# Optimization experiments

Hardware: AMD Instinct MI355X
Metric: run time of the kernel (lower is better)

## Reference

```python
import jax, jax.numpy as jnp
import numpy as np

B, N, C = 64, 1024, 128
H1, H2 = 256, 128
ACTION = N


def _xavier(key, shape):
    lim = float(np.sqrt(6.0 / (shape[0] + shape[1])))
    return jax.random.uniform(key, shape, jnp.float32, -lim, lim)


def setup_inputs() -> dict:
    key = jax.random.key(0)
    ks = jax.random.split(key, 16)
    node_features = jax.random.normal(ks[0], (B, N, 3), jnp.float32)
    adjacency_matrix = jax.random.randint(ks[1], (B, N, N), 0, 2).astype(jnp.int32)
    return {
        "node_features": node_features,
        "adjacency_matrix": adjacency_matrix,
        "W_in": _xavier(ks[2], (3, C)),
        "a_src": _xavier(ks[3], (C, 1)),
        "a_dst": _xavier(ks[4], (C, 1)),
        "a_src2": _xavier(ks[5], (C, 1)),
        "a_dst2": _xavier(ks[6], (C, 1)),
        "W1": _xavier(ks[7], (C, H1)),
        "b1": jnp.zeros((H1,), jnp.float32),
        "W2": _xavier(ks[8], (H1, H2)),
        "b2": jnp.zeros((H2,), jnp.float32),
        "Wpi": _xavier(ks[9], (H2, ACTION)),
        "bpi": jnp.zeros((ACTION,), jnp.float32),
        "Wv": _xavier(ks[10], (H2, 1)),
        "bv": jnp.zeros((1,), jnp.float32),
    }


def _gat_layer(x, mask, a_src, a_dst):
    # x: [B,N,C]; mask: [B,N,N] bool
    ai = jnp.squeeze(x @ a_src, -1)  # [B,N] score of node as source (i)
    aj = jnp.squeeze(x @ a_dst, -1)  # [B,N] score of node as dest (j)
    e = ai[:, :, None] + aj[:, None, :]  # [B,N,N]
    e = jnp.where(e > 0, e, 0.2 * e)  # leaky_relu(0.2)
    e = jnp.where(mask, e, jnp.float32(-1e9))  # masked_fill(-inf)
    alpha = jax.nn.softmax(e, axis=-1)  # [B,N,N]
    out = jnp.einsum("bij,bjc->bic", alpha, x)  # weighted neighbor aggregation
    return jax.nn.relu(out)


def reference(node_features, adjacency_matrix, W_in, a_src, a_dst, a_src2, a_dst2,
              W1, b1, W2, b2, Wpi, bpi, Wv, bv):
    mask = adjacency_matrix > 0
    x = node_features @ W_in  # [B,N,C], no bias
    x = _gat_layer(x, mask, a_src, a_dst)
    x = _gat_layer(x, mask, a_src2, a_dst2)
    x = jnp.mean(x, axis=1)  # [B,C]
    x = jax.nn.relu(x @ W1 + b1)
    x = jax.nn.relu(x @ W2 + b2)
    pi = jax.nn.softmax(x @ Wpi + bpi, axis=1)
    v = x @ Wv + bv
    return (pi, v)
```

## Files before the change

kernel.cpp:

```cpp
#include <hip/hip_runtime.h>

#define Bn 64
#define Nn 1024
#define Cc 128

typedef _Float16 h8 __attribute__((ext_vector_type(8)));
typedef float f4v __attribute__((ext_vector_type(4)));
typedef unsigned long long u64;

__global__ __launch_bounds__(256) void k_feat(
    const float* __restrict__ nf, const float* __restrict__ Win,
    const float* __restrict__ asrc, const float* __restrict__ adst,
    _Float16* __restrict__ X0, float* __restrict__ ai, float* __restrict__ aj,
    float* __restrict__ E, float* __restrict__ G, float* __restrict__ F, float* __restrict__ H) {
  int g = blockIdx.x; int b = g >> 7; int n0 = (g & 127) << 3;
  int t = threadIdx.x; int c = t >> 1; int h = t & 1;
  float w0 = Win[c], w1 = Win[Cc + c], w2 = Win[2 * Cc + c];
  float as_ = asrc[c], ad = adst[c];
  float ps[4], pd[4];
  _Float16 hv[4];
  #pragma unroll
  for (int r = 0; r < 4; r++) {
    int n = n0 + (h << 2) + r;
    const float* p = nf + ((size_t)(b << 10) + n) * 3;
    float x = p[0] * w0 + p[1] * w1 + p[2] * w2;
    hv[r] = (_Float16)x; ps[r] = x * as_; pd[r] = x * ad;
  }
  *(uint2*)(X0 + ((size_t)b << 17) + ((size_t)(g & 127) << 10) + (c << 3) + (h << 2)) = *(uint2*)hv;
  #pragma unroll
  for (int off = 32; off > 1; off >>= 1) {
    #pragma unroll
    for (int r = 0; r < 4; r++) { ps[r] += __shfl_down(ps[r], off, 64); pd[r] += __shfl_down(pd[r], off, 64); }
  }
  __shared__ float red[4][2][4][2];
  int lane = t & 63, wv = t >> 6;
  if (lane < 2) {
    #pragma unroll
    for (int r = 0; r < 4; r++) { red[wv][lane][r][0] = ps[r]; red[wv][lane][r][1] = pd[r]; }
  }
  __syncthreads();
  if (t < 8) {
    int hh = t >> 2, r = t & 3;
    float sa = 0.f, sd = 0.f;
    #pragma unroll
    for (int w = 0; w < 4; w++) { sa += red[w][hh][r][0]; sd += red[w][hh][r][1]; }
    int gi = (b << 10) + n0 + t;
    ai[gi] = sa; aj[gi] = sd;
    E[gi] = __expf(sa); G[gi] = __expf(0.2f * sa);
    F[gi] = __expf(sd); H[gi] = __expf(0.2f * sd);
  }
}

__global__ __launch_bounds__(256) void k_scores2(
    const _Float16* __restrict__ X1,
    const float* __restrict__ asrc, const float* __restrict__ adst,
    float* __restrict__ ai, float* __restrict__ aj,
    float* __restrict__ E, float* __restrict__ G, float* __restrict__ F, float* __restrict__ H) {
  int g = blockIdx.x; int b = g >> 7; int n0 = (g & 127) << 3;
  int t = threadIdx.x; int c = t >> 1; int h = t & 1;
  float as_ = asrc[c], ad = adst[c];
  uint2 raw = *(const uint2*)(X1 + ((size_t)b << 17) + ((size_t)(g & 127) << 10) + (c << 3) + (h << 2));
  const _Float16* hp = (const _Float16*)&raw;
  float ps[4], pd[4];
  #pragma unroll
  for (int r = 0; r < 4; r++) { float x = (float)hp[r]; ps[r] = x * as_; pd[r] = x * ad; }
  #pragma unroll
  for (int off = 32; off > 1; off >>= 1) {
    #pragma unroll
    for (int r = 0; r < 4; r++) { ps[r] += __shfl_down(ps[r], off, 64); pd[r] += __shfl_down(pd[r], off, 64); }
  }
  __shared__ float red[4][2][4][2];
  int lane = t & 63, wv = t >> 6;
  if (lane < 2) {
    #pragma unroll
    for (int r = 0; r < 4; r++) { red[wv][lane][r][0] = ps[r]; red[wv][lane][r][1] = pd[r]; }
  }
  __syncthreads();
  if (t < 8) {
    int hh = t >> 2, r = t & 3;
    float sa = 0.f, sd = 0.f;
    #pragma unroll
    for (int w = 0; w < 4; w++) { sa += red[w][hh][r][0]; sd += red[w][hh][r][1]; }
    int gi = (b << 10) + n0 + t;
    ai[gi] = sa; aj[gi] = sd;
    E[gi] = __expf(sa); G[gi] = __expf(0.2f * sa);
    F[gi] = __expf(sd); H[gi] = __expf(0.2f * sd);
  }
}

template <int LAYER>
__global__ __launch_bounds__(256, 4) void k_agg(
    const _Float16* __restrict__ X, const int* __restrict__ adj,
    const float* __restrict__ ai, const float* __restrict__ E, const float* __restrict__ G,
    const float* __restrict__ aj, const float* __restrict__ F, const float* __restrict__ H,
    u64* __restrict__ pm, _Float16* __restrict__ Y, float* __restrict__ xmp) {
  __shared__ __align__(16) char smem[34304];
  _Float16* sB = (_Float16*)smem;
  _Float16* sA = (_Float16*)(smem + 8192);
  float* s_aj = (float*)(smem + 12288);
  float* s_F  = (float*)(smem + 16384);
  float* s_H  = (float*)(smem + 20480);
  unsigned char* s_pm = (unsigned char*)(smem + 24576);
  float* tile = (float*)smem;

  const int b = blockIdx.y, i0 = blockIdx.x << 6;
  const int tid = threadIdx.x;
  const int lane = tid & 63, wv = tid >> 6;
  const int m = lane & 15, quad = lane >> 4;
  const int wi = wv >> 1, wc = wv & 1;
  const int gbase = b << 10;

  ((float4*)s_aj)[tid] = ((const float4*)(aj + gbase))[tid];
  ((float4*)s_F)[tid]  = ((const float4*)(F + gbase))[tid];
  ((float4*)s_H)[tid]  = ((const float4*)(H + gbase))[tid];

  if (LAYER == 1) {
    ushort* pmu = (ushort*)pm;
    #pragma unroll 2
    for (int pass = 0; pass < 16; ++pass) {
      int r = (wv << 4) + pass;
      const uint4* arow = (const uint4*)(adj + ((size_t)(gbase + i0 + r) << 10));
      uint4 v0 = arow[(lane << 2) | 0], v1 = arow[(lane << 2) | 1];
      uint4 v2 = arow[(lane << 2) | 2], v3 = arow[(lane << 2) | 3];
      unsigned int bits =
          (v0.x) | (v0.y << 1) | (v0.z << 2) | (v0.w << 3) |
          (v1.x << 4) | (v1.y << 5) | (v1.z << 6) | (v1.w << 7) |
          (v2.x << 8) | (v2.y << 9) | (v2.z << 10) | (v2.w << 11) |
          (v3.x << 12) | (v3.y << 13) | (v3.z << 14) | (v3.w << 15);
      *(ushort*)(s_pm + r * 152 + (lane << 1)) = (ushort)bits;
      pmu[((size_t)(gbase + i0 + r) << 6) + lane] = (ushort)bits;
    }
  } else {
    const u64* pmg = pm + (((size_t)(gbase + i0)) << 4);
    #pragma unroll
    for (int k = tid; k < 1024; k += 256) {
      int r = k >> 4, w = k & 15;
      *(u64*)(s_pm + r * 152 + (w << 3)) = pmg[k];
    }
  }

  const int gi = gbase + i0 + lane;
  const float ai_i = ai[gi];
  const float Ed = E[gi], Gd = G[gi];
  float dsum = 0.f;

  f4v acc[2][4];
  #pragma unroll
  for (int a = 0; a < 2; a++)
    #pragma unroll
    for (int ct = 0; ct < 4; ct++) { f4v z = {0.f, 0.f, 0.f, 0.f}; acc[a][ct] = z; }

  const char* xb = (const char*)(X + ((size_t)b << 17));
  __syncthreads();

  for (int kt = 0; kt < 32; ++kt) {
    const int jt = kt << 5;
    const char* gsrc = xb + (jt << 8) + (wv << 11) + lane * 16;
    uint4 r0 = *(const uint4*)gsrc;
    uint4 r1 = *(const uint4*)(gsrc + 1024);
    h8 af;
    {
      const int j0 = jt + (wv << 3);
      float aw[8], fw[8], hw[8];
      *(float4*)&aw[0] = *(const float4*)&s_aj[j0]; *(float4*)&aw[4] = *(const float4*)&s_aj[j0 + 4];
      *(float4*)&fw[0] = *(const float4*)&s_F[j0];  *(float4*)&fw[4] = *(const float4*)&s_F[j0 + 4];
      *(float4*)&hw[0] = *(const float4*)&s_H[j0];  *(float4*)&hw[4] = *(const float4*)&s_H[j0 + 4];
      unsigned int mbyte = s_pm[lane * 152 + (jt >> 3) + wv];
      #pragma unroll
      for (int jj = 0; jj < 8; jj++) {
        float e = ai_i + aw[jj];
        bool pos = e > 0.f;
        float wi_ = pos ? Ed : Gd;
        float wj_ = pos ? fw[jj] : hw[jj];
        float val = ((mbyte >> jj) & 1u) ? wi_ * wj_ : 0.f;
        dsum += val;
        af[jj] = (_Float16)val;
      }
    }
    __syncthreads();
    {
      char* ldst = (char*)sB + (wv << 11) + lane * 16;
      *(uint4*)ldst = r0;
      *(uint4*)(ldst + 1024) = r1;
      *((h8*)sA + (wv << 6) + lane) = af;
    }
    __syncthreads();
    {
      const h8* pA = (const h8*)sA;
      const h8* pB = (const h8*)sB;
      h8 a0 = pA[(quad << 6) + (wi << 5) + m];
      h8 a1 = pA[(quad << 6) + (wi << 5) + 16 + m];
      #pragma unroll
      for (int ct = 0; ct < 4; ct++) {
        h8 bf = pB[(quad << 7) + (wc << 6) + (ct << 4) + m];
        acc[0][ct] = __builtin_amdgcn_mfma_f32_16x16x32_f16(a0, bf, acc[0][ct], 0, 0, 0);
        acc[1][ct] = __builtin_amdgcn_mfma_f32_16x16x32_f16(a1, bf, acc[1][ct], 0, 0, 0);
      }
    }
  }
  __syncthreads();
  float* dsum_s = (float*)(smem + 12288);
  dsum_s[(lane << 2) + wv] = dsum;
  __syncthreads();
  float rd8[2][4];
  #pragma unroll
  for (int a = 0; a < 2; a++)
    #pragma unroll
    for (int r = 0; r < 4; r++) {
      int lr = (wi << 5) + (a << 4) + (quad << 2) + r;
      float4 d4 = *(const float4*)&dsum_s[lr << 2];
      rd8[a][r] = 1.0f / ((d4.x + d4.y) + (d4.z + d4.w));
    }
  __syncthreads();
  #pragma unroll
  for (int a = 0; a < 2; a++)
    #pragma unroll
    for (int ct = 0; ct < 4; ct++)
      #pragma unroll
      for (int r = 0; r < 4; r++) {
        int lr = (wi << 5) + (a << 4) + (quad << 2) + r;
        int c = (wc << 6) + (ct << 4) + m;
        tile[lr * 132 + c] = fmaxf(acc[a][ct][r] * rd8[a][r], 0.f);
      }
  __syncthreads();
  if (LAYER == 1) {
    _Float16 hv[32];
    #pragma unroll
    for (int s = 0; s < 32; s++) {
      int q = (tid << 5) + s;
      int li = ((q >> 10) << 3) + (q & 7), c = (q >> 3) & 127;
      hv[s] = (_Float16)tile[li * 132 + c];
    }
    uint4* o = (uint4*)(Y + ((size_t)b << 17) + ((size_t)i0 << 7) + (tid << 5));
    o[0] = *(uint4*)&hv[0]; o[1] = *(uint4*)&hv[8];
    o[2] = *(uint4*)&hv[16]; o[3] = *(uint4*)&hv[24];
  } else {
    if (tid < 128) {
      float s = 0.f;
      #pragma unroll
      for (int i = 0; i < 64; i++) s += tile[i * 132 + tid];
      xmp[(((b << 4) + blockIdx.x) << 7) + tid] = s;
    }
  }
}

__global__ __launch_bounds__(256) void k_head(
    const float* __restrict__ xmp, const float* __restrict__ W1, const float* __restrict__ b1,
    const float* __restrict__ W2, const float* __restrict__ b2,
    const float* __restrict__ Wpi, const float* __restrict__ bpi,
    const float* __restrict__ Wv, const float* __restrict__ bv,
    float* __restrict__ out) {
  int b = blockIdx.x, t = threadIdx.x;
  __shared__ float xs[128], h1[256], h2[128], red[4];
  if (t < 128) {
    const float* p = xmp + ((size_t)b << 11);
    float s = 0.f;
    #pragma unroll
    for (int xb = 0; xb < 16; xb++) s += p[(xb << 7) + t];
    xs[t] = s * (1.f / 1024.f);
  }
  __syncthreads();
  float s = 0.f;
  #pragma unroll 8
  for (int k = 0; k < 128; k++) s += xs[k] * W1[k * 256 + t];
  h1[t] = fmaxf(s + b1[t], 0.f);
  __syncthreads();
  if (t < 128) {
    float s2 = 0.f;
    #pragma unroll 8
    for (int k = 0; k < 256; k++) s2 += h1[k] * W2[k * 128 + t];
    h2[t] = fmaxf(s2 + b2[t], 0.f);
  }
  __syncthreads();
  float lg[4];
  #pragma unroll
  for (int q = 0; q < 4; q++) {
    int o = t + (q << 8);
    float s3 = 0.f;
    #pragma unroll 8
    for (int k = 0; k < 128; k++) s3 += h2[k] * Wpi[k * 1024 + o];
    lg[q] = s3 + bpi[o];
  }
  float mx = fmaxf(fmaxf(lg[0], lg[1]), fmaxf(lg[2], lg[3]));
  #pragma unroll
  for (int off = 32; off > 0; off >>= 1) mx = fmaxf(mx, __shfl_down(mx, off, 64));
  if ((t & 63) == 0) red[t >> 6] = mx;
  __syncthreads();
  mx = fmaxf(fmaxf(red[0], red[1]), fmaxf(red[2], red[3]));
  __syncthreads();
  float ex[4]; float sum = 0.f;
  #pragma unroll
  for (int q = 0; q < 4; q++) { ex[q] = __expf(lg[q] - mx); sum += ex[q]; }
  #pragma unroll
  for (int off = 32; off > 0; off >>= 1) sum += __shfl_down(sum, off, 64);
  if ((t & 63) == 0) red[t >> 6] = sum;
  __syncthreads();
  sum = red[0] + red[1] + red[2] + red[3];
  float rs = 1.0f / sum;
  #pragma unroll
  for (int q = 0; q < 4; q++) out[((size_t)b << 10) + t + (q << 8)] = ex[q] * rs;
  __syncthreads();
  float vp = (t < 128) ? h2[t] * Wv[t] : 0.f;
  #pragma unroll
  for (int off = 32; off > 0; off >>= 1) vp += __shfl_down(vp, off, 64);
  if ((t & 63) == 0) red[t >> 6] = vp;
  __syncthreads();
  if (t == 0) out[65536 + b] = red[0] + red[1] + red[2] + red[3] + bv[0];
}

extern "C" void kernel_launch(void* const* d_in, const int* in_sizes, int n_in,
                              void* d_out, int out_size, void* d_ws, size_t ws_size,
                              hipStream_t stream) {
  const float* nf    = (const float*)d_in[0];
  const int*   adj   = (const int*)  d_in[1];
  const float* Win   = (const float*)d_in[2];
  const float* asrc  = (const float*)d_in[3];
  const float* adst  = (const float*)d_in[4];
  const float* asrc2 = (const float*)d_in[5];
  const float* adst2 = (const float*)d_in[6];
  const float* W1    = (const float*)d_in[7];
  const float* b1    = (const float*)d_in[8];
  const float* W2    = (const float*)d_in[9];
  const float* b2    = (const float*)d_in[10];
  const float* Wpi   = (const float*)d_in[11];
  const float* bpi   = (const float*)d_in[12];
  const float* Wv    = (const float*)d_in[13];
  const float* bv    = (const float*)d_in[14];
  float* out = (float*)d_out;

  char* ws = (char*)d_ws;
  _Float16* x0 = (_Float16*)(ws);
  _Float16* x1 = (_Float16*)(ws + 16777216);
  u64* pm = (u64*)(ws + 33554432);
  char* S = ws + 41943040;
  float* ai1 = (float*)(S + 0 * 262144);
  float* aj1 = (float*)(S + 1 * 262144);
  float* E1  = (float*)(S + 2 * 262144);
  float* G1  = (float*)(S + 3 * 262144);
  float* F1  = (float*)(S + 4 * 262144);
  float* H1  = (float*)(S + 5 * 262144);
  float* ai2 = (float*)(S + 6 * 262144);
  float* aj2 = (float*)(S + 7 * 262144);
  float* E2  = (float*)(S + 8 * 262144);
  float* G2  = (float*)(S + 9 * 262144);
  float* F2  = (float*)(S + 10 * 262144);
  float* H2  = (float*)(S + 11 * 262144);
  float* xmp = (float*)(S + 12 * 262144);

  k_feat<<<8192, 256, 0, stream>>>(nf, Win, asrc, adst, x0, ai1, aj1, E1, G1, F1, H1);
  dim3 ag(16, Bn);
  k_agg<1><<<ag, 256, 0, stream>>>(x0, adj, ai1, E1, G1, aj1, F1, H1, pm, x1, nullptr);
  k_scores2<<<8192, 256, 0, stream>>>(x1, asrc2, adst2, ai2, aj2, E2, G2, F2, H2);
  k_agg<2><<<ag, 256, 0, stream>>>(x1, nullptr, ai2, E2, G2, aj2, F2, H2, pm, nullptr, xmp);
  k_head<<<Bn, 256, 0, stream>>>(xmp, W1, b1, W2, b2, Wpi, bpi, Wv, bv, out);
}
```

Baseline: 547.6 us.

## Compute attention weights and B fragments in registers, drop LDS staging

Each wave now computes its own A fragments (attention weights for its rows) directly in MFMA register layout and loads X fragments straight from global memory into registers, which removes the per-iteration LDS staging and both __syncthreads in the main loop. Row sums are reduced with cross-lane shuffles instead of shared memory. The cost is redundant weight computation across the two column-split waves, uncoalesced 16-byte global loads per lane, and a lowered occupancy hint (4 to 3 blocks) to allow more registers.

```diff
diff --git a/kernel.cpp b/kernel.cpp
--- a/kernel.cpp
+++ b/kernel.cpp
@@ -89,18 +89,16 @@
 }
 
 template <int LAYER>
-__global__ __launch_bounds__(256, 4) void k_agg(
+__global__ __launch_bounds__(256, 3) void k_agg(
     const _Float16* __restrict__ X, const int* __restrict__ adj,
     const float* __restrict__ ai, const float* __restrict__ E, const float* __restrict__ G,
     const float* __restrict__ aj, const float* __restrict__ F, const float* __restrict__ H,
     u64* __restrict__ pm, _Float16* __restrict__ Y, float* __restrict__ xmp) {
-  __shared__ __align__(16) char smem[34304];
-  _Float16* sB = (_Float16*)smem;
-  _Float16* sA = (_Float16*)(smem + 8192);
-  float* s_aj = (float*)(smem + 12288);
-  float* s_F  = (float*)(smem + 16384);
-  float* s_H  = (float*)(smem + 20480);
-  unsigned char* s_pm = (unsigned char*)(smem + 24576);
+  __shared__ __align__(16) char smem[33792];
+  float* s_aj = (float*)smem;
+  float* s_F  = (float*)(smem + 4096);
+  float* s_H  = (float*)(smem + 8192);
+  unsigned char* s_pm = (unsigned char*)(smem + 12288);
   float* tile = (float*)smem;
 
   const int b = blockIdx.y, i0 = blockIdx.x << 6;
@@ -139,10 +137,11 @@
     }
   }
 
-  const int gi = gbase + i0 + lane;
-  const float ai_i = ai[gi];
-  const float Ed = E[gi], Gd = G[gi];
-  float dsum = 0.f;
+  const int r0 = (wi << 5) + m;
+  const int gi0 = gbase + i0 + r0;
+  const float ai0 = ai[gi0],      E0c = E[gi0],      G0c = G[gi0];
+  const float ai1 = ai[gi0 + 16], E1c = E[gi0 + 16], G1c = G[gi0 + 16];
+  float dsum0 = 0.f, dsum1 = 0.f;
 
   f4v acc[2][4];
   #pragma unroll
@@ -150,67 +149,60 @@
     #pragma unroll
     for (int ct = 0; ct < 4; ct++) { f4v z = {0.f, 0.f, 0.f, 0.f}; acc[a][ct] = z; }
 
-  const char* xb = (const char*)(X + ((size_t)b << 17));
+  const char* gB = (const char*)(X + ((size_t)b << 17)) + (((quad << 7) + (wc << 6) + m) << 4);
+  const unsigned char* pmr0 = s_pm + r0 * 152;
+  const unsigned char* pmr1 = pmr0 + 16 * 152;
+
   __syncthreads();
 
   for (int kt = 0; kt < 32; ++kt) {
-    const int jt = kt << 5;
-    const char* gsrc = xb + (jt << 8) + (wv << 11) + lane * 16;
-    uint4 r0 = *(const uint4*)gsrc;
-    uint4 r1 = *(const uint4*)(gsrc + 1024);
-    h8 af;
-    {
-      const int j0 = jt + (wv << 3);
-      float aw[8], fw[8], hw[8];
-      *(float4*)&aw[0] = *(const float4*)&s_aj[j0]; *(float4*)&aw[4] = *(const float4*)&s_aj[j0 + 4];
-      *(float4*)&fw[0] = *(const float4*)&s_F[j0];  *(float4*)&fw[4] = *(const float4*)&s_F[j0 + 4];
-      *(float4*)&hw[0] = *(const float4*)&s_H[j0];  *(float4*)&hw[4] = *(const float4*)&s_H[j0 + 4];
-      unsigned int mbyte = s_pm[lane * 152 + (jt >> 3) + wv];
-      #pragma unroll
-      for (int jj = 0; jj < 8; jj++) {
-        float e = ai_i + aw[jj];
-        bool pos = e > 0.f;
-        float wi_ = pos ? Ed : Gd;
-        float wj_ = pos ? fw[jj] : hw[jj];
-        float val = ((mbyte >> jj) & 1u) ? wi_ * wj_ : 0.f;
-        dsum += val;
-        af[jj] = (_Float16)val;
-      }
-    }
-    __syncthreads();
-    {
-      char* ldst = (char*)sB + (wv << 11) + lane * 16;
-      *(uint4*)ldst = r0;
-      *(uint4*)(ldst + 1024) = r1;
-      *((h8*)sA + (wv << 6) + lane) = af;
-    }
-    __syncthreads();
-    {
-      const h8* pA = (const h8*)sA;
-      const h8* pB = (const h8*)sB;
-      h8 a0 = pA[(quad << 6) + (wi << 5) + m];
-      h8 a1 = pA[(quad << 6) + (wi << 5) + 16 + m];
-      #pragma unroll
-      for (int ct = 0; ct < 4; ct++) {
-        h8 bf = pB[(quad << 7) + (wc << 6) + (ct << 4) + m];
-        acc[0][ct] = __builtin_amdgcn_mfma_f32_16x16x32_f16(a0, bf, acc[0][ct], 0, 0, 0);
-        acc[1][ct] = __builtin_amdgcn_mfma_f32_16x16x32_f16(a1, bf, acc[1][ct], 0, 0, 0);
-      }
-    }
-  }
-  __syncthreads();
-  float* dsum_s = (float*)(smem + 12288);
-  dsum_s[(lane << 2) + wv] = dsum;
-  __syncthreads();
+    h8 b0 = *(const h8*)(gB);
+    h8 b1 = *(const h8*)(gB + 256);
+    h8 b2 = *(const h8*)(gB + 512);
+    h8 b3 = *(const h8*)(gB + 768);
+    gB += 8192;
+    const int j0 = (kt << 5) + (quad << 3);
+    float aw[8], fw[8], hw[8];
+    *(float4*)&aw[0] = *(const float4*)&s_aj[j0]; *(float4*)&aw[4] = *(const float4*)&s_aj[j0 + 4];
+    *(float4*)&fw[0] = *(const float4*)&s_F[j0];  *(float4*)&fw[4] = *(const float4*)&s_F[j0 + 4];
+    *(float4*)&hw[0] = *(const float4*)&s_H[j0];  *(float4*)&hw[4] = *(const float4*)&s_H[j0 + 4];
+    unsigned int mb0 = pmr0[(kt << 2) + quad];
+    unsigned int mb1 = pmr1[(kt << 2) + quad];
+    h8 a0, a1;
+    #pragma unroll
+    for (int e = 0; e < 8; e++) {
+      float ew = aw[e], fe = fw[e], he = hw[e];
+      bool p0 = (ai0 + ew) > 0.f;
+      float v0 = (p0 ? E0c : G0c) * (p0 ? fe : he);
+      v0 = ((mb0 >> e) & 1u) ? v0 : 0.f;
+      dsum0 += v0; a0[e] = (_Float16)v0;
+      bool p1 = (ai1 + ew) > 0.f;
+      float v1 = (p1 ? E1c : G1c) * (p1 ? fe : he);
+      v1 = ((mb1 >> e) & 1u) ? v1 : 0.f;
+      dsum1 += v1; a1[e] = (_Float16)v1;
+    }
+    acc[0][0] = __builtin_amdgcn_mfma_f32_16x16x32_f16(a0, b0, acc[0][0], 0, 0, 0);
+    acc[1][0] = __builtin_amdgcn_mfma_f32_16x16x32_f16(a1, b0, acc[1][0], 0, 0, 0);
+    acc[0][1] = __builtin_amdgcn_mfma_f32_16x16x32_f16(a0, b1, acc[0][1], 0, 0, 0);
+    acc[1][1] = __builtin_amdgcn_mfma_f32_16x16x32_f16(a1, b1, acc[1][1], 0, 0, 0);
+    acc[0][2] = __builtin_amdgcn_mfma_f32_16x16x32_f16(a0, b2, acc[0][2], 0, 0, 0);
+    acc[1][2] = __builtin_amdgcn_mfma_f32_16x16x32_f16(a1, b2, acc[1][2], 0, 0, 0);
+    acc[0][3] = __builtin_amdgcn_mfma_f32_16x16x32_f16(a0, b3, acc[0][3], 0, 0, 0);
+    acc[1][3] = __builtin_amdgcn_mfma_f32_16x16x32_f16(a1, b3, acc[1][3], 0, 0, 0);
+  }
+
+  dsum0 += __shfl_xor(dsum0, 16, 64);
+  dsum0 += __shfl_xor(dsum0, 32, 64);
+  dsum1 += __shfl_xor(dsum1, 16, 64);
+  dsum1 += __shfl_xor(dsum1, 32, 64);
   float rd8[2][4];
   #pragma unroll
-  for (int a = 0; a < 2; a++)
-    #pragma unroll
-    for (int r = 0; r < 4; r++) {
-      int lr = (wi << 5) + (a << 4) + (quad << 2) + r;
-      float4 d4 = *(const float4*)&dsum_s[lr << 2];
-      rd8[a][r] = 1.0f / ((d4.x + d4.y) + (d4.z + d4.w));
-    }
+  for (int r = 0; r < 4; r++) {
+    int src = (quad << 2) + r;
+    rd8[0][r] = 1.0f / __shfl(dsum0, src, 64);
+    rd8[1][r] = 1.0f / __shfl(dsum1, src, 64);
+  }
+
   __syncthreads();
   #pragma unroll
   for (int a = 0; a < 2; a++)
```

After: 573.4 us. 1.05x slower.
